# Performance work log

Hardware: AMD Instinct MI355X
Metric: run time of the kernel (lower is better)

Reference implementation:

```python
import jax, jax.numpy as jnp
from jax import lax
import numpy as np

CONF_THRES = 0.25
IOU_THRES = 0.45
MAX_WH = 7680.0   # per-class box offset (yolov5 agnostic=False trick)
TOP_K = 5000      # pre-NMS candidate cap (yolov5 uses max_nms=30000; capped for tractable IoU matrix)


def _xywh2xyxy(b):
    xy, wh = b[..., :2], b[..., 2:4]
    half = wh * 0.5
    return jnp.concatenate([xy - half, xy + half], axis=-1)


def _box_iou(a, b):
    # a: [K,4], b: [K,4] xyxy -> [K,K]
    area_a = (a[:, 2] - a[:, 0]) * (a[:, 3] - a[:, 1])
    area_b = (b[:, 2] - b[:, 0]) * (b[:, 3] - b[:, 1])
    lt = jnp.maximum(a[:, None, :2], b[None, :, :2])
    rb = jnp.minimum(a[:, None, 2:], b[None, :, 2:])
    wh = jnp.clip(rb - lt, 0.0)
    inter = wh[..., 0] * wh[..., 1]
    return inter / (area_a[:, None] + area_b[None, :] - inter + 1e-7)


def _nms_single(pred_i, max_det):
    # pred_i: [N, 5+nc] = (x, y, w, h, obj, cls...)
    obj = pred_i[:, 4]
    cls_conf = pred_i[:, 5:] * obj[:, None]          # conf = obj * cls
    score = jnp.max(cls_conf, axis=-1)                # best class (multi_label=False)
    cls = jnp.argmax(cls_conf, axis=-1).astype(pred_i.dtype)
    boxes = _xywh2xyxy(pred_i[:, :4])
    valid = (obj > CONF_THRES) & (score > CONF_THRES)
    mscore = jnp.where(valid, score, -1.0)

    # pre-NMS top-k candidates by confidence (yolov5 sorts by conf)
    top_s, idx = lax.top_k(mscore, TOP_K)
    tb = boxes[idx]                                   # [K,4]
    tc = cls[idx]                                     # [K]
    tvalid = top_s > 0.0

    # offset boxes by class so different classes never suppress each other
    ob = tb + (tc * MAX_WH)[:, None]
    iou = lax.stop_gradient(_box_iou(ob, ob))         # [K,K]
    ar = jnp.arange(TOP_K)

    def step(keep, i):
        sup = keep[i] & (iou[i] > IOU_THRES) & (ar > i)
        return keep & ~sup, None

    keep, _ = lax.scan(step, tvalid, ar)
    keep = keep & tvalid

    fscore = jnp.where(keep, top_s, -1.0)
    fs, fi = lax.top_k(fscore, max_det)
    det = jnp.concatenate([tb[fi], top_s[fi][:, None], tc[fi][:, None]], axis=-1)  # [max_det, 6]
    return jnp.where((fs > 0.0)[:, None], det, 0.0)


def setup_inputs() -> dict:
    key = jax.random.key(0)
    k1, k2, k3, k4 = jax.random.split(key, 4)
    B, N, NC = 8, 25200, 80
    xy = jax.random.uniform(k1, (B, N, 2)) * 608.0 + 16.0
    wh = jax.random.uniform(k2, (B, N, 2)) * 120.0 + 8.0
    obj = jax.random.uniform(k3, (B, N, 1))
    cls = jax.random.uniform(k4, (B, N, NC))
    pred = jnp.concatenate([xy, wh, obj, cls], axis=-1).astype(jnp.float32)
    return {"pred": pred, "max_det": 300}


def reference(pred, max_det):
    # pred: [B, N, 5+nc] -> detections [B, max_det, 6] = (x1, y1, x2, y2, conf, cls)
    return jax.vmap(lambda p: _nms_single(p, max_det))(pred)
```

## Files before the change

### kernel.cpp

```cpp
#include <hip/hip_runtime.h>

typedef unsigned long long ull;

#define N_PRED 25200
#define NCLS   80
#define ROWW   85
#define TOPK   5000
#define IOU_T  0.45f
#define MAXWH  7680.0f

#define K2T    1024
#define MAXE   25
#define CAP    512
#define CAPB   256
#define PTPB   256
#define PROWS  128
#define K4T    1024
#define MAXE4  5
#define SELN   320

__device__ __forceinline__ int SIX(int d) { return d + (d >> 5); }

__device__ __forceinline__ void scan_find(const unsigned* hist, int nb, unsigned k, ull* sbd) {
  const int l = (int)threadIdx.x;
  const int bpl = nb >> 6;
  unsigned s = 0;
  for (int j = 0; j < bpl; ++j) s += hist[SIX(l * bpl + j)];
  unsigned suf = s;
  #pragma unroll
  for (int o = 1; o < 64; o <<= 1) {
    unsigned t = __shfl_down(suf, (unsigned)o, 64);
    if (l + o < 64) suf += t;
  }
  unsigned sufN = __shfl_down(suf, 1u, 64);
  if (l == 63) sufN = 0;
  if (suf >= k && sufN < k) {
    unsigned cum = sufN;
    for (int j = bpl - 1; j >= 0; --j) {
      unsigned c = hist[SIX(l * bpl + j)];
      if (cum + c >= k) { sbd[0] = (ull)(l * bpl + j); sbd[1] = (ull)(k - cum); break; }
      cum += c;
    }
  }
}

__global__ __launch_bounds__(1024) void zero_kernel(unsigned* __restrict__ z, int nwords) {
  int i = blockIdx.x * 1024 + (int)threadIdx.x;
  if (i < nwords) z[i] = 0u;
}

__global__ __launch_bounds__(PTPB) void prep_kernel(const float* __restrict__ pred,
    ull* __restrict__ pk, float4* __restrict__ boxes, float* __restrict__ clsf,
    unsigned* __restrict__ ghist) {
  __shared__ float sr[PROWS * ROWW];
  __shared__ unsigned hist[2048];
  const int b = blockIdx.y;
  const int rbase = blockIdx.x * PROWS;
  int nrows = N_PRED - rbase; if (nrows > PROWS) nrows = PROWS;
  const int tid = (int)threadIdx.x;
  for (int i = tid; i < 2048; i += PTPB) hist[i] = 0;
  const float* src = pred + ((size_t)b * N_PRED + rbase) * ROWW;
  const int nfl4 = (nrows * ROWW) >> 2;
  for (int i = tid; i < nfl4; i += PTPB) {
    float4 t; __builtin_memcpy(&t, src + i * 4, 16);
    *(float4*)&sr[i * 4] = t;
  }
  __syncthreads();
  const int r = tid >> 1, h = tid & 1;
  if (r < nrows) {
    const float* row = sr + r * ROWW;
    float obj = row[4];
    float best = -1.0f; int bi = 0;
    const int c0 = h * 40;
    for (int c = 0; c < 40; ++c) {
      float p = __fmul_rn(row[5 + c0 + c], obj);
      if (p > best) { best = p; bi = c0 + c; }
    }
    float ob_ = __shfl_xor(best, 1, 64);
    int   oi  = __shfl_xor(bi, 1, 64);
    if (h == 0) {
      if (!(best >= ob_)) { best = ob_; bi = oi; }
      bool valid = (obj > 0.25f) && (best > 0.25f);
      float ms = valid ? best : -1.0f;
      unsigned kb = __float_as_uint(ms);
      kb = (kb & 0x80000000u) ? ~kb : (kb | 0x80000000u);
      const int g = rbase + r;
      pk[(size_t)b * N_PRED + g] = ((ull)kb << 32) | (unsigned)~(unsigned)g;
      float x = row[0], y = row[1], w = row[2], hh2 = row[3];
      float hw = __fmul_rn(w, 0.5f), hh = __fmul_rn(hh2, 0.5f);
      boxes[(size_t)b * N_PRED + g] = make_float4(__fsub_rn(x, hw), __fsub_rn(y, hh),
                                                  __fadd_rn(x, hw), __fadd_rn(y, hh));
      clsf[(size_t)b * N_PRED + g] = (float)bi;
      atomicAdd(&hist[kb >> 21], 1u);
    }
  }
  __syncthreads();
  for (int i = tid; i < 2048; i += PTPB) {
    unsigned cn = hist[i];
    if (cn) atomicAdd(&ghist[b * 2048 + i], cn);
  }
}

__global__ __launch_bounds__(K2T) void thresh_kernel(const ull* __restrict__ pkArr,
    const unsigned* __restrict__ ghist, const float* __restrict__ clsf,
    ull* __restrict__ bucket, unsigned* __restrict__ bucketCnt) {
  __shared__ unsigned hist[2112];
  __shared__ ull sbd[2];
  const int b = blockIdx.x;
  const int tid = (int)threadIdx.x;
  ull v[MAXE];
  #pragma unroll
  for (int e = 0; e < MAXE; ++e) {
    int i = tid + e * K2T;
    v[e] = (i < N_PRED) ? pkArr[(size_t)b * N_PRED + i] : 0ull;
  }
  unsigned k = TOPK;
  ull pfx = 0;
  for (int i = tid; i < 2048; i += K2T) hist[SIX(i)] = ghist[b * 2048 + i];
  __syncthreads();
  if (tid < 64) scan_find(hist, 2048, k, sbd);
  __syncthreads();
  {
    ull d = sbd[0]; unsigned kp = (unsigned)sbd[1];
    unsigned c = hist[SIX((int)d)];
    pfx |= d << 53; k = kp;
    if (kp != c) {
      const int shifts[5] = {42, 31, 20, 9, 0};
      const int widths[5] = {11, 11, 11, 11, 9};
      for (int p = 0; p < 5; ++p) {
        const int sh = shifts[p];
        const int nb = 1 << widths[p];
        __syncthreads();
        for (int i = tid; i < 2112; i += K2T) hist[i] = 0;
        __syncthreads();
        const int hb = sh + widths[p];
        const ull hm = ~((1ull << hb) - 1ull);
        #pragma unroll
        for (int e = 0; e < MAXE; ++e) {
          ull pv = v[e];
          if ((pv & hm) == pfx)
            atomicAdd(&hist[SIX((int)((pv >> sh) & (ull)(nb - 1)))], 1u);
        }
        __syncthreads();
        if (tid < 64) scan_find(hist, nb, k, sbd);
        __syncthreads();
        ull d2 = sbd[0]; unsigned kp2 = (unsigned)sbd[1];
        unsigned c2 = hist[SIX((int)d2)];
        pfx |= d2 << sh; k = kp2;
        if (kp2 == c2) break;
      }
    }
  }
  const ull thr = pfx;
  #pragma unroll
  for (int e = 0; e < MAXE; ++e) {
    ull pv = v[e];
    if (pv >= thr) {
      unsigned idx = ~(unsigned)(pv & 0xFFFFFFFFull);
      int c = (int)clsf[(size_t)b * N_PRED + idx];
      unsigned pos = atomicAdd(&bucketCnt[b * NCLS + c], 1u);
      if (pos < CAP) bucket[((size_t)b * NCLS + c) * CAP + pos] = pv;
    }
  }
}

__global__ __launch_bounds__(64) void nms_kernel(const ull* __restrict__ bucket,
    const unsigned* __restrict__ bucketCnt, const float4* __restrict__ boxes,
    ull* __restrict__ keptPk, float4* __restrict__ keptBox, float2* __restrict__ keptSC,
    unsigned* __restrict__ keptCnt) {
  const int c = blockIdx.x, b = blockIdx.y, lane = (int)threadIdx.x;
  __shared__ ull su[CAPB];
  __shared__ ull spk[CAPB];
  __shared__ float4 sob[CAPB];
  unsigned kxu = bucketCnt[b * NCLS + c];
  int kx = (kxu > CAPB) ? CAPB : (int)kxu;
  if (kx == 0) return;
  const float cf = (float)c;
  const float off = __fmul_rn(cf, MAXWH);
  const ull* bk = bucket + ((size_t)b * NCLS + c) * CAP;
  for (int i = lane; i < kx; i += 64) su[i] = bk[i];
  __syncthreads();
  {
    ull mine[4]; int rk[4] = {0, 0, 0, 0};
    #pragma unroll
    for (int r = 0; r < 4; ++r) mine[r] = (r * 64 + lane < kx) ? su[r * 64 + lane] : 0ull;
    for (int j = 0; j < kx; ++j) {
      ull x = su[j];
      #pragma unroll
      for (int r = 0; r < 4; ++r) rk[r] += (x > mine[r]) ? 1 : 0;
    }
    #pragma unroll
    for (int r = 0; r < 4; ++r)
      if (r * 64 + lane < kx) spk[rk[r]] = mine[r];
  }
  __syncthreads();
  for (int i = lane; i < kx; i += 64) {
    unsigned idx = ~(unsigned)(spk[i] & 0xFFFFFFFFull);
    float4 bx = boxes[(size_t)b * N_PRED + idx];
    sob[i] = make_float4(__fadd_rn(bx.x, off), __fadd_rn(bx.y, off),
                         __fadd_rn(bx.z, off), __fadd_rn(bx.w, off));
  }
  __syncthreads();
  ull rowm[4][4] = {{0ull}};
  #pragma unroll
  for (int r = 0; r < 4; ++r) {
    if (r * 64 < kx) {
      const int i = r * 64 + lane;
      const bool act = i < kx;
      float4 A = sob[act ? i : 0];
      float areaA = __fmul_rn(__fsub_rn(A.z, A.x), __fsub_rn(A.w, A.y));
      #pragma unroll
      for (int w = 0; w < 4; ++w) {
        if (w >= r && w * 64 < kx) {
          ull m = 0ull;
          int jmax = kx - w * 64; if (jmax > 64) jmax = 64;
          for (int jj = 0; jj < jmax; ++jj) {
            const int j = w * 64 + jj;
            float4 Bx = sob[j];
            float areaB = __fmul_rn(__fsub_rn(Bx.z, Bx.x), __fsub_rn(Bx.w, Bx.y));
            float wx = fmaxf(__fsub_rn(fminf(A.z, Bx.z), fmaxf(A.x, Bx.x)), 0.0f);
            float wy = fmaxf(__fsub_rn(fminf(A.w, Bx.w), fmaxf(A.y, Bx.y)), 0.0f);
            float inter = __fmul_rn(wx, wy);
            float denom = __fadd_rn(__fsub_rn(__fadd_rn(areaA, areaB), inter), 1e-7f);
            float iou = __fdiv_rn(inter, denom);
            if (act && j > i && iou > IOU_T) m |= 1ull << jj;
          }
          rowm[r][w] = m;
        }
      }
    }
  }
  ull alive[4];
  #pragma unroll
  for (int w = 0; w < 4; ++w) {
    int rem = kx - w * 64;
    alive[w] = (rem >= 64) ? ~0ull : (rem > 0 ? ((1ull << rem) - 1ull) : 0ull);
  }
  #pragma unroll
  for (int w = 0; w < 4; ++w) {
    if (w * 64 < kx) {
      int bmax = kx - w * 64; if (bmax > 64) bmax = 64;
      for (int bit = 0; bit < bmax; ++bit) {
        if ((alive[w] >> bit) & 1ull) {
          #pragma unroll
          for (int w2 = 0; w2 < 4; ++w2) {
            if (w2 >= w && w2 * 64 < kx) {
              ull row = __shfl(rowm[w][w2], bit, 64);
              alive[w2] &= ~row;
            }
          }
        }
      }
    }
  }
  int tot = 0;
  #pragma unroll
  for (int w = 0; w < 4; ++w) tot += (int)__popcll(alive[w]);
  unsigned gbase = 0;
  if (lane == 0) gbase = atomicAdd(&keptCnt[b], (unsigned)tot);
  gbase = __shfl(gbase, 0, 64);
  unsigned pre = 0;
  #pragma unroll
  for (int w = 0; w < 4; ++w) {
    if (w * 64 < kx) {
      ull aw = alive[w];
      int i = w * 64 + lane;
      bool kp = (i < kx) && ((aw >> lane) & 1ull);
      if (kp) {
        unsigned pos = gbase + pre + (unsigned)__popcll(aw & ((1ull << lane) - 1ull));
        if (pos < TOPK) {
          ull p = spk[i];
          unsigned idx = ~(unsigned)(p & 0xFFFFFFFFull);
          keptPk[(size_t)b * TOPK + pos] = p;
          keptBox[(size_t)b * TOPK + pos] = boxes[(size_t)b * N_PRED + idx];
          keptSC[(size_t)b * TOPK + pos] =
              make_float2(__uint_as_float((unsigned)(p >> 32) & 0x7FFFFFFFu), cf);
        }
      }
      pre += (unsigned)__popcll(aw);
    }
  }
}

__global__ __launch_bounds__(K4T) void out_kernel(const ull* __restrict__ keptPk,
    const float4* __restrict__ keptBox, const float2* __restrict__ keptSC,
    const unsigned* __restrict__ keptCnt, float* __restrict__ out, int maxdet) {
  __shared__ unsigned hist[2112];
  __shared__ ull sbd[2];
  __shared__ ull sPk[SELN];
  __shared__ int sSlot[SELN];
  __shared__ unsigned scnt;
  const int b = blockIdx.x;
  const int tid = (int)threadIdx.x;
  float* ob = out + (size_t)b * maxdet * 6;
  for (int i = tid; i < maxdet * 6; i += K4T) ob[i] = 0.0f;
  const unsigned K = keptCnt[b];
  const unsigned kk = (K < (unsigned)maxdet) ? K : (unsigned)maxdet;
  if (kk == 0) return;
  ull v[MAXE4];
  #pragma unroll
  for (int e = 0; e < MAXE4; ++e) {
    unsigned i = (unsigned)tid + e * K4T;
    v[e] = (i < K) ? keptPk[(size_t)b * TOPK + i] : 0ull;
  }
  ull thr = 1ull;
  if (K > (unsigned)maxdet) {
    unsigned k = kk;
    ull pfx = 0;
    const int shifts[6] = {53, 42, 31, 20, 9, 0};
    const int widths[6] = {11, 11, 11, 11, 11, 9};
    for (int p = 0; p < 6; ++p) {
      const int sh = shifts[p];
      const int nb = 1 << widths[p];
      for (int i = tid; i < 2112; i += K4T) hist[i] = 0;
      __syncthreads();
      const int hb = sh + widths[p];
      const ull hm = (hb >= 64) ? 0ull : ~((1ull << hb) - 1ull);
      #pragma unroll
      for (int e = 0; e < MAXE4; ++e) {
        ull pv = v[e];
        if (pv != 0ull && (pv & hm) == pfx)
          atomicAdd(&hist[SIX((int)((pv >> sh) & (ull)(nb - 1)))], 1u);
      }
      __syncthreads();
      if (tid < 64) scan_find(hist, nb, k, sbd);
      __syncthreads();
      ull d = sbd[0]; unsigned kp = (unsigned)sbd[1];
      unsigned c = hist[SIX((int)d)];
      pfx |= d << sh; k = kp;
      if (kp == c) break;
      __syncthreads();
    }
    thr = pfx;
  }
  if (tid == 0) scnt = 0;
  __syncthreads();
  const int lane = tid & 63;
  #pragma unroll
  for (int e = 0; e < MAXE4; ++e) {
    unsigned i = (unsigned)tid + e * K4T;
    bool sel = (i < K) && (v[e] >= thr);
    ull m = __ballot(sel);
    if (m) {
      unsigned basep = 0;
      if (lane == 0) basep = atomicAdd(&scnt, (unsigned)__popcll(m));
      basep = __shfl(basep, 0, 64);
      if (sel) {
        unsigned pos = basep + (unsigned)__popcll(m & ((1ull << lane) - 1ull));
        if (pos < SELN) { sPk[pos] = v[e]; sSlot[pos] = (int)i; }
      }
    }
  }
  __syncthreads();
  const int n = (int)scnt;
  for (int i = tid; i < n; i += K4T) {
    ull mypk = sPk[i];
    int rank = 0;
    for (int j = 0; j < n; ++j) rank += (sPk[j] > mypk) ? 1 : 0;
    if (rank < maxdet) {
      int slot = sSlot[i];
      float4 bx = keptBox[(size_t)b * TOPK + slot];
      float2 sc = keptSC[(size_t)b * TOPK + slot];
      float* dst = ob + (size_t)rank * 6;
      dst[0] = bx.x; dst[1] = bx.y; dst[2] = bx.z; dst[3] = bx.w;
      dst[4] = sc.x; dst[5] = sc.y;
    }
  }
}

extern "C" void kernel_launch(void* const* d_in, const int* in_sizes, int n_in,
                              void* d_out, int out_size, void* d_ws, size_t ws_size,
                              hipStream_t stream) {
  const float* pred = (const float*)d_in[0];
  const int B = in_sizes[0] / (N_PRED * ROWW);
  const int maxdet = out_size / (B * 6);

  char* p = (char*)d_ws;
  auto carve = [&](size_t bytes) { char* r = p; p += (bytes + 255) & ~(size_t)255; return (void*)r; };
  ull*      pk      = (ull*)carve((size_t)B * N_PRED * 8);
  float4*   boxes   = (float4*)carve((size_t)B * N_PRED * 16);
  float*    clsf    = (float*)carve((size_t)B * N_PRED * 4);
  size_t zbytes = (size_t)B * 2048 * 4 + (size_t)B * NCLS * 4 + (size_t)B * 4;
  char*     zbase     = (char*)carve(zbytes);
  unsigned* ghist     = (unsigned*)zbase;
  unsigned* bucketCnt = (unsigned*)(zbase + (size_t)B * 2048 * 4);
  unsigned* keptCnt   = (unsigned*)(zbase + (size_t)B * 2048 * 4 + (size_t)B * NCLS * 4);
  ull*      bucket  = (ull*)carve((size_t)B * NCLS * CAP * 8);
  ull*      keptPk  = (ull*)carve((size_t)B * TOPK * 8);
  float4*   keptBox = (float4*)carve((size_t)B * TOPK * 16);
  float2*   keptSC  = (float2*)carve((size_t)B * TOPK * 8);

  const int nwords = (int)(zbytes / 4);
  zero_kernel<<<(nwords + 1023) / 1024, 1024, 0, stream>>>((unsigned*)zbase, nwords);
  prep_kernel<<<dim3((N_PRED + PROWS - 1) / PROWS, B), PTPB, 0, stream>>>(pred, pk, boxes, clsf, ghist);
  thresh_kernel<<<B, K2T, 0, stream>>>(pk, ghist, clsf, bucket, bucketCnt);
  nms_kernel<<<dim3(NCLS, B), 64, 0, stream>>>(bucket, bucketCnt, boxes,
                                               keptPk, keptBox, keptSC, keptCnt);
  out_kernel<<<B, K4T, 0, stream>>>(keptPk, keptBox, keptSC, keptCnt, (float*)d_out, maxdet);
}
```

Baseline: 113.0 us.

## Widen global histogram, drop box/class arrays, recompute boxes from pred in NMS

```diff
diff --git a/kernel.cpp b/kernel.cpp
--- a/kernel.cpp
+++ b/kernel.cpp
@@ -14,10 +14,12 @@
 #define CAP    512
 #define CAPB   256
 #define PTPB   256
-#define PROWS  128
+#define PROWS  64
+#define NHBIN  32768
 #define K4T    1024
 #define MAXE4  5
 #define SELN   320
+#define SENT   0xFFFFFFFFull
 
 __device__ __forceinline__ int SIX(int d) { return d + (d >> 5); }
 
@@ -50,15 +52,12 @@
 }
 
 __global__ __launch_bounds__(PTPB) void prep_kernel(const float* __restrict__ pred,
-    ull* __restrict__ pk, float4* __restrict__ boxes, float* __restrict__ clsf,
-    unsigned* __restrict__ ghist) {
+    ull* __restrict__ pk, unsigned char* __restrict__ cls8, unsigned* __restrict__ ghist) {
   __shared__ float sr[PROWS * ROWW];
-  __shared__ unsigned hist[2048];
   const int b = blockIdx.y;
   const int rbase = blockIdx.x * PROWS;
   int nrows = N_PRED - rbase; if (nrows > PROWS) nrows = PROWS;
   const int tid = (int)threadIdx.x;
-  for (int i = tid; i < 2048; i += PTPB) hist[i] = 0;
   const float* src = pred + ((size_t)b * N_PRED + rbase) * ROWW;
   const int nfl4 = (nrows * ROWW) >> 2;
   for (int i = tid; i < nfl4; i += PTPB) {
@@ -66,44 +65,47 @@
     *(float4*)&sr[i * 4] = t;
   }
   __syncthreads();
-  const int r = tid >> 1, h = tid & 1;
+  const int r = tid >> 2, q = tid & 3;
   if (r < nrows) {
     const float* row = sr + r * ROWW;
     float obj = row[4];
     float best = -1.0f; int bi = 0;
-    const int c0 = h * 40;
-    for (int c = 0; c < 40; ++c) {
+    const int c0 = q * 20;
+    for (int c = 0; c < 20; ++c) {
       float p = __fmul_rn(row[5 + c0 + c], obj);
       if (p > best) { best = p; bi = c0 + c; }
     }
-    float ob_ = __shfl_xor(best, 1, 64);
-    int   oi  = __shfl_xor(bi, 1, 64);
-    if (h == 0) {
-      if (!(best >= ob_)) { best = ob_; bi = oi; }
+    {
+      float obq = __shfl_xor(best, 1, 64); int oiq = __shfl_xor(bi, 1, 64);
+      bool lo = (q & 1) == 0;
+      float aB = lo ? best : obq; int aI = lo ? bi : oiq;
+      float bB = lo ? obq : best; int bI = lo ? oiq : bi;
+      if (aB >= bB) { best = aB; bi = aI; } else { best = bB; bi = bI; }
+    }
+    {
+      float obq = __shfl_xor(best, 2, 64); int oiq = __shfl_xor(bi, 2, 64);
+      bool lo = (q & 2) == 0;
+      float aB = lo ? best : obq; int aI = lo ? bi : oiq;
+      float bB = lo ? obq : best; int bI = lo ? oiq : bi;
+      if (aB >= bB) { best = aB; bi = aI; } else { best = bB; bi = bI; }
+    }
+    if (q == 0) {
       bool valid = (obj > 0.25f) && (best > 0.25f);
       float ms = valid ? best : -1.0f;
       unsigned kb = __float_as_uint(ms);
       kb = (kb & 0x80000000u) ? ~kb : (kb | 0x80000000u);
       const int g = rbase + r;
       pk[(size_t)b * N_PRED + g] = ((ull)kb << 32) | (unsigned)~(unsigned)g;
-      float x = row[0], y = row[1], w = row[2], hh2 = row[3];
-      float hw = __fmul_rn(w, 0.5f), hh = __fmul_rn(hh2, 0.5f);
-      boxes[(size_t)b * N_PRED + g] = make_float4(__fsub_rn(x, hw), __fsub_rn(y, hh),
-                                                  __fadd_rn(x, hw), __fadd_rn(y, hh));
-      clsf[(size_t)b * N_PRED + g] = (float)bi;
-      atomicAdd(&hist[kb >> 21], 1u);
-    }
-  }
-  __syncthreads();
-  for (int i = tid; i < 2048; i += PTPB) {
-    unsigned cn = hist[i];
-    if (cn) atomicAdd(&ghist[b * 2048 + i], cn);
+      cls8[(size_t)b * N_PRED + g] = (unsigned char)bi;
+      if (valid) atomicAdd(&ghist[b * NHBIN + (kb >> 17)], 1u);
+    }
   }
 }
 
 __global__ __launch_bounds__(K2T) void thresh_kernel(const ull* __restrict__ pkArr,
-    const unsigned* __restrict__ ghist, const float* __restrict__ clsf,
+    const unsigned* __restrict__ ghist, const unsigned char* __restrict__ cls8,
     ull* __restrict__ bucket, unsigned* __restrict__ bucketCnt) {
+  __shared__ unsigned ssum[1024];
   __shared__ unsigned hist[2112];
   __shared__ ull sbd[2];
   const int b = blockIdx.x;
@@ -114,19 +116,53 @@
     int i = tid + e * K2T;
     v[e] = (i < N_PRED) ? pkArr[(size_t)b * N_PRED + i] : 0ull;
   }
-  unsigned k = TOPK;
-  ull pfx = 0;
-  for (int i = tid; i < 2048; i += K2T) hist[SIX(i)] = ghist[b * 2048 + i];
-  __syncthreads();
-  if (tid < 64) scan_find(hist, 2048, k, sbd);
-  __syncthreads();
-  {
-    ull d = sbd[0]; unsigned kp = (unsigned)sbd[1];
-    unsigned c = hist[SIX((int)d)];
-    pfx |= d << 53; k = kp;
-    if (kp != c) {
-      const int shifts[5] = {42, 31, 20, 9, 0};
-      const int widths[5] = {11, 11, 11, 11, 9};
+  const unsigned* g = ghist + (size_t)b * NHBIN;
+  if (tid == 0) { sbd[0] = SENT; }
+  unsigned tsum = 0;
+  #pragma unroll 4
+  for (int j = 0; j < 32; ++j) tsum += g[tid * 32 + j];
+  ssum[tid] = tsum;
+  __syncthreads();
+  if (tid < 64) {
+    unsigned ls = 0;
+    for (int j = 0; j < 16; ++j) ls += ssum[tid * 16 + j];
+    unsigned suf = ls;
+    #pragma unroll
+    for (int o = 1; o < 64; o <<= 1) {
+      unsigned t = __shfl_down(suf, (unsigned)o, 64);
+      if (tid + o < 64) suf += t;
+    }
+    unsigned sufN = __shfl_down(suf, 1u, 64);
+    if (tid == 63) sufN = 0;
+    if (suf >= (unsigned)TOPK && sufN < (unsigned)TOPK) {
+      unsigned cum = sufN;
+      for (int j = 15; j >= 0; --j) {
+        unsigned c = ssum[tid * 16 + j];
+        if (cum + c >= (unsigned)TOPK) { sbd[0] = (ull)(tid * 16 + j); sbd[1] = (ull)((unsigned)TOPK - cum); break; }
+        cum += c;
+      }
+    }
+  }
+  __syncthreads();
+  if ((ull)tid == sbd[0]) {
+    unsigned krem = (unsigned)sbd[1], cum2 = 0;
+    for (int j = 31; j >= 0; --j) {
+      unsigned c = g[tid * 32 + j];
+      if (cum2 + c >= krem) { sbd[0] = (ull)(tid * 32 + j); sbd[1] = (ull)(krem - cum2); break; }
+      cum2 += c;
+    }
+  }
+  __syncthreads();
+  ull thr;
+  if (sbd[0] == SENT) {
+    thr = 1ull << 63;
+  } else {
+    ull pfx = sbd[0] << 49;
+    unsigned k = (unsigned)sbd[1];
+    unsigned cnt0 = g[(int)sbd[0]];
+    if (k != cnt0) {
+      const int shifts[5] = {38, 27, 16, 5, 0};
+      const int widths[5] = {11, 11, 11, 11, 5};
       for (int p = 0; p < 5; ++p) {
         const int sh = shifts[p];
         const int nb = 1 << widths[p];
@@ -150,14 +186,14 @@
         if (kp2 == c2) break;
       }
     }
-  }
-  const ull thr = pfx;
+    thr = pfx;
+  }
   #pragma unroll
   for (int e = 0; e < MAXE; ++e) {
     ull pv = v[e];
     if (pv >= thr) {
       unsigned idx = ~(unsigned)(pv & 0xFFFFFFFFull);
-      int c = (int)clsf[(size_t)b * N_PRED + idx];
+      int c = (int)cls8[(size_t)b * N_PRED + idx];
       unsigned pos = atomicAdd(&bucketCnt[b * NCLS + c], 1u);
       if (pos < CAP) bucket[((size_t)b * NCLS + c) * CAP + pos] = pv;
     }
@@ -165,13 +201,14 @@
 }
 
 __global__ __launch_bounds__(64) void nms_kernel(const ull* __restrict__ bucket,
-    const unsigned* __restrict__ bucketCnt, const float4* __restrict__ boxes,
+    const unsigned* __restrict__ bucketCnt, const float* __restrict__ pred,
     ull* __restrict__ keptPk, float4* __restrict__ keptBox, float2* __restrict__ keptSC,
     unsigned* __restrict__ keptCnt) {
   const int c = blockIdx.x, b = blockIdx.y, lane = (int)threadIdx.x;
   __shared__ ull su[CAPB];
   __shared__ ull spk[CAPB];
   __shared__ float4 sob[CAPB];
+  __shared__ float4 srb[CAPB];
   unsigned kxu = bucketCnt[b * NCLS + c];
   int kx = (kxu > CAPB) ? CAPB : (int)kxu;
   if (kx == 0) return;
@@ -196,9 +233,13 @@
   __syncthreads();
   for (int i = lane; i < kx; i += 64) {
     unsigned idx = ~(unsigned)(spk[i] & 0xFFFFFFFFull);
-    float4 bx = boxes[(size_t)b * N_PRED + idx];
-    sob[i] = make_float4(__fadd_rn(bx.x, off), __fadd_rn(bx.y, off),
-                         __fadd_rn(bx.z, off), __fadd_rn(bx.w, off));
+    float4 t0; __builtin_memcpy(&t0, pred + ((size_t)b * N_PRED + idx) * ROWW, 16);
+    float hw = __fmul_rn(t0.z, 0.5f), hh = __fmul_rn(t0.w, 0.5f);
+    float4 rb = make_float4(__fsub_rn(t0.x, hw), __fsub_rn(t0.y, hh),
+                            __fadd_rn(t0.x, hw), __fadd_rn(t0.y, hh));
+    srb[i] = rb;
+    sob[i] = make_float4(__fadd_rn(rb.x, off), __fadd_rn(rb.y, off),
+                         __fadd_rn(rb.z, off), __fadd_rn(rb.w, off));
   }
   __syncthreads();
   ull rowm[4][4] = {{0ull}};
@@ -270,9 +311,8 @@
         unsigned pos = gbase + pre + (unsigned)__popcll(aw & ((1ull << lane) - 1ull));
         if (pos < TOPK) {
           ull p = spk[i];
-          unsigned idx = ~(unsigned)(p & 0xFFFFFFFFull);
           keptPk[(size_t)b * TOPK + pos] = p;
-          keptBox[(size_t)b * TOPK + pos] = boxes[(size_t)b * N_PRED + idx];
+          keptBox[(size_t)b * TOPK + pos] = srb[i];
           keptSC[(size_t)b * TOPK + pos] =
               make_float2(__uint_as_float((unsigned)(p >> 32) & 0x7FFFFFFFu), cf);
         }
@@ -293,9 +333,9 @@
   const int b = blockIdx.x;
   const int tid = (int)threadIdx.x;
   float* ob = out + (size_t)b * maxdet * 6;
-  for (int i = tid; i < maxdet * 6; i += K4T) ob[i] = 0.0f;
   const unsigned K = keptCnt[b];
   const unsigned kk = (K < (unsigned)maxdet) ? K : (unsigned)maxdet;
+  for (int i = (int)kk * 6 + tid; i < maxdet * 6; i += K4T) ob[i] = 0.0f;
   if (kk == 0) return;
   ull v[MAXE4];
   #pragma unroll
@@ -377,14 +417,13 @@
 
   char* p = (char*)d_ws;
   auto carve = [&](size_t bytes) { char* r = p; p += (bytes + 255) & ~(size_t)255; return (void*)r; };
-  ull*      pk      = (ull*)carve((size_t)B * N_PRED * 8);
-  float4*   boxes   = (float4*)carve((size_t)B * N_PRED * 16);
-  float*    clsf    = (float*)carve((size_t)B * N_PRED * 4);
-  size_t zbytes = (size_t)B * 2048 * 4 + (size_t)B * NCLS * 4 + (size_t)B * 4;
+  ull*           pk     = (ull*)carve((size_t)B * N_PRED * 8);
+  unsigned char* cls8   = (unsigned char*)carve((size_t)B * N_PRED);
+  size_t zbytes = (size_t)B * NHBIN * 4 + (size_t)B * NCLS * 4 + (size_t)B * 4;
   char*     zbase     = (char*)carve(zbytes);
   unsigned* ghist     = (unsigned*)zbase;
-  unsigned* bucketCnt = (unsigned*)(zbase + (size_t)B * 2048 * 4);
-  unsigned* keptCnt   = (unsigned*)(zbase + (size_t)B * 2048 * 4 + (size_t)B * NCLS * 4);
+  unsigned* bucketCnt = (unsigned*)(zbase + (size_t)B * NHBIN * 4);
+  unsigned* keptCnt   = (unsigned*)(zbase + (size_t)B * NHBIN * 4 + (size_t)B * NCLS * 4);
   ull*      bucket  = (ull*)carve((size_t)B * NCLS * CAP * 8);
   ull*      keptPk  = (ull*)carve((size_t)B * TOPK * 8);
   float4*   keptBox = (float4*)carve((size_t)B * TOPK * 16);
@@ -392,9 +431,9 @@
 
   const int nwords = (int)(zbytes / 4);
   zero_kernel<<<(nwords + 1023) / 1024, 1024, 0, stream>>>((unsigned*)zbase, nwords);
-  prep_kernel<<<dim3((N_PRED + PROWS - 1) / PROWS, B), PTPB, 0, stream>>>(pred, pk, boxes, clsf, ghist);
-  thresh_kernel<<<B, K2T, 0, stream>>>(pk, ghist, clsf, bucket, bucketCnt);
-  nms_kernel<<<dim3(NCLS, B), 64, 0, stream>>>(bucket, bucketCnt, boxes,
+  prep_kernel<<<dim3((N_PRED + PROWS - 1) / PROWS, B), PTPB, 0, stream>>>(pred, pk, cls8, ghist);
+  thresh_kernel<<<B, K2T, 0, stream>>>(pk, ghist, cls8, bucket, bucketCnt);
+  nms_kernel<<<dim3(NCLS, B), 64, 0, stream>>>(bucket, bucketCnt, pred,
                                                keptPk, keptBox, keptSC, keptCnt);
   out_kernel<<<B, K4T, 0, stream>>>(keptPk, keptBox, keptSC, keptCnt, (float*)d_out, maxdet);
 }
```

Result: slower. 157.7 us (+39.5%).

## Drop full-size box and class arrays; recompute boxes from pred for candidates

Applied to the files above, without the earlier changes.

```diff
diff --git a/kernel.cpp b/kernel.cpp
--- a/kernel.cpp
+++ b/kernel.cpp
@@ -50,8 +50,7 @@
 }
 
 __global__ __launch_bounds__(PTPB) void prep_kernel(const float* __restrict__ pred,
-    ull* __restrict__ pk, float4* __restrict__ boxes, float* __restrict__ clsf,
-    unsigned* __restrict__ ghist) {
+    ull* __restrict__ pk, unsigned char* __restrict__ cls8, unsigned* __restrict__ ghist) {
   __shared__ float sr[PROWS * ROWW];
   __shared__ unsigned hist[2048];
   const int b = blockIdx.y;
@@ -86,11 +85,7 @@
       kb = (kb & 0x80000000u) ? ~kb : (kb | 0x80000000u);
       const int g = rbase + r;
       pk[(size_t)b * N_PRED + g] = ((ull)kb << 32) | (unsigned)~(unsigned)g;
-      float x = row[0], y = row[1], w = row[2], hh2 = row[3];
-      float hw = __fmul_rn(w, 0.5f), hh = __fmul_rn(hh2, 0.5f);
-      boxes[(size_t)b * N_PRED + g] = make_float4(__fsub_rn(x, hw), __fsub_rn(y, hh),
-                                                  __fadd_rn(x, hw), __fadd_rn(y, hh));
-      clsf[(size_t)b * N_PRED + g] = (float)bi;
+      cls8[(size_t)b * N_PRED + g] = (unsigned char)bi;
       atomicAdd(&hist[kb >> 21], 1u);
     }
   }
@@ -102,7 +97,7 @@
 }
 
 __global__ __launch_bounds__(K2T) void thresh_kernel(const ull* __restrict__ pkArr,
-    const unsigned* __restrict__ ghist, const float* __restrict__ clsf,
+    const unsigned* __restrict__ ghist, const unsigned char* __restrict__ cls8,
     ull* __restrict__ bucket, unsigned* __restrict__ bucketCnt) {
   __shared__ unsigned hist[2112];
   __shared__ ull sbd[2];
@@ -155,9 +150,9 @@
   #pragma unroll
   for (int e = 0; e < MAXE; ++e) {
     ull pv = v[e];
-    if (pv >= thr) {
+    if (pv >= thr && (pv >> 63)) {
       unsigned idx = ~(unsigned)(pv & 0xFFFFFFFFull);
-      int c = (int)clsf[(size_t)b * N_PRED + idx];
+      int c = (int)cls8[(size_t)b * N_PRED + idx];
       unsigned pos = atomicAdd(&bucketCnt[b * NCLS + c], 1u);
       if (pos < CAP) bucket[((size_t)b * NCLS + c) * CAP + pos] = pv;
     }
@@ -165,13 +160,14 @@
 }
 
 __global__ __launch_bounds__(64) void nms_kernel(const ull* __restrict__ bucket,
-    const unsigned* __restrict__ bucketCnt, const float4* __restrict__ boxes,
+    const unsigned* __restrict__ bucketCnt, const float* __restrict__ pred,
     ull* __restrict__ keptPk, float4* __restrict__ keptBox, float2* __restrict__ keptSC,
     unsigned* __restrict__ keptCnt) {
   const int c = blockIdx.x, b = blockIdx.y, lane = (int)threadIdx.x;
   __shared__ ull su[CAPB];
   __shared__ ull spk[CAPB];
   __shared__ float4 sob[CAPB];
+  __shared__ float4 srb[CAPB];
   unsigned kxu = bucketCnt[b * NCLS + c];
   int kx = (kxu > CAPB) ? CAPB : (int)kxu;
   if (kx == 0) return;
@@ -196,9 +192,13 @@
   __syncthreads();
   for (int i = lane; i < kx; i += 64) {
     unsigned idx = ~(unsigned)(spk[i] & 0xFFFFFFFFull);
-    float4 bx = boxes[(size_t)b * N_PRED + idx];
-    sob[i] = make_float4(__fadd_rn(bx.x, off), __fadd_rn(bx.y, off),
-                         __fadd_rn(bx.z, off), __fadd_rn(bx.w, off));
+    float4 t0; __builtin_memcpy(&t0, pred + ((size_t)b * N_PRED + idx) * ROWW, 16);
+    float hw = __fmul_rn(t0.z, 0.5f), hh = __fmul_rn(t0.w, 0.5f);
+    float4 rb = make_float4(__fsub_rn(t0.x, hw), __fsub_rn(t0.y, hh),
+                            __fadd_rn(t0.x, hw), __fadd_rn(t0.y, hh));
+    srb[i] = rb;
+    sob[i] = make_float4(__fadd_rn(rb.x, off), __fadd_rn(rb.y, off),
+                         __fadd_rn(rb.z, off), __fadd_rn(rb.w, off));
   }
   __syncthreads();
   ull rowm[4][4] = {{0ull}};
@@ -270,9 +270,8 @@
         unsigned pos = gbase + pre + (unsigned)__popcll(aw & ((1ull << lane) - 1ull));
         if (pos < TOPK) {
           ull p = spk[i];
-          unsigned idx = ~(unsigned)(p & 0xFFFFFFFFull);
           keptPk[(size_t)b * TOPK + pos] = p;
-          keptBox[(size_t)b * TOPK + pos] = boxes[(size_t)b * N_PRED + idx];
+          keptBox[(size_t)b * TOPK + pos] = srb[i];
           keptSC[(size_t)b * TOPK + pos] =
               make_float2(__uint_as_float((unsigned)(p >> 32) & 0x7FFFFFFFu), cf);
         }
@@ -293,9 +292,9 @@
   const int b = blockIdx.x;
   const int tid = (int)threadIdx.x;
   float* ob = out + (size_t)b * maxdet * 6;
-  for (int i = tid; i < maxdet * 6; i += K4T) ob[i] = 0.0f;
   const unsigned K = keptCnt[b];
   const unsigned kk = (K < (unsigned)maxdet) ? K : (unsigned)maxdet;
+  for (int i = (int)kk * 6 + tid; i < maxdet * 6; i += K4T) ob[i] = 0.0f;
   if (kk == 0) return;
   ull v[MAXE4];
   #pragma unroll
@@ -377,9 +376,8 @@
 
   char* p = (char*)d_ws;
   auto carve = [&](size_t bytes) { char* r = p; p += (bytes + 255) & ~(size_t)255; return (void*)r; };
-  ull*      pk      = (ull*)carve((size_t)B * N_PRED * 8);
-  float4*   boxes   = (float4*)carve((size_t)B * N_PRED * 16);
-  float*    clsf    = (float*)carve((size_t)B * N_PRED * 4);
+  ull*           pk   = (ull*)carve((size_t)B * N_PRED * 8);
+  unsigned char* cls8 = (unsigned char*)carve((size_t)B * N_PRED);
   size_t zbytes = (size_t)B * 2048 * 4 + (size_t)B * NCLS * 4 + (size_t)B * 4;
   char*     zbase     = (char*)carve(zbytes);
   unsigned* ghist     = (unsigned*)zbase;
@@ -392,9 +390,9 @@
 
   const int nwords = (int)(zbytes / 4);
   zero_kernel<<<(nwords + 1023) / 1024, 1024, 0, stream>>>((unsigned*)zbase, nwords);
-  prep_kernel<<<dim3((N_PRED + PROWS - 1) / PROWS, B), PTPB, 0, stream>>>(pred, pk, boxes, clsf, ghist);
-  thresh_kernel<<<B, K2T, 0, stream>>>(pk, ghist, clsf, bucket, bucketCnt);
-  nms_kernel<<<dim3(NCLS, B), 64, 0, stream>>>(bucket, bucketCnt, boxes,
+  prep_kernel<<<dim3((N_PRED + PROWS - 1) / PROWS, B), PTPB, 0, stream>>>(pred, pk, cls8, ghist);
+  thresh_kernel<<<B, K2T, 0, stream>>>(pk, ghist, cls8, bucket, bucketCnt);
+  nms_kernel<<<dim3(NCLS, B), 64, 0, stream>>>(bucket, bucketCnt, pred,
                                                keptPk, keptBox, keptSC, keptCnt);
   out_kernel<<<B, K4T, 0, stream>>>(keptPk, keptBox, keptSC, keptCnt, (float*)d_out, maxdet);
 }
```

Result: no change. 111.9 us (-1.0%).
